# Optimization experiments

Measured on AMD Instinct MI355X. Metric: run time of the kernel, lower is better.

Reference implementation:

```python
import jax, jax.numpy as jnp
import numpy as np
from jax import lax

NUM_NEURONS = 144
NUM_E = 115  # int(144 * 0.8)
NEURONS_PER_CELL = 16
TAU = 2.0
V_TH = 1.0

# action -> (dx, dy) -> grid cell -> neuron slice; precomputed 5x144 current table
_ACTION_TO_POS = {0: (1, 0), 1: (0, -1), 2: (-1, 0), 3: (0, 1), 4: (0, 0)}

def _build_action_table():
    tab = np.zeros((5, NUM_NEURONS), dtype=np.float32)
    for a, (dx, dy) in _ACTION_TO_POS.items():
        x, y = 1 + dx, 1 + dy
        if 0 <= x < 3 and 0 <= y < 3:
            cell = y * 3 + x
            tab[a, cell * NEURONS_PER_CELL:(cell + 1) * NEURONS_PER_CELL] = 5.0
    return jnp.asarray(tab)

_EI_MASK = jnp.concatenate([jnp.ones(NUM_E, jnp.float32), -jnp.ones(NUM_NEURONS - NUM_E, jnp.float32)])


def setup_inputs() -> dict:
    key = jax.random.key(0)
    k1, k2, k3, k4 = jax.random.split(key, 4)
    B, NB = 16384, 8
    actions = jax.random.randint(k1, (B,), 0, 5)
    neighbor_E_spikes = (jax.random.uniform(k2, (B, NB, NUM_E)) < 0.2).astype(jnp.float32)
    W_rec = jax.random.normal(k3, (NUM_NEURONS, NUM_NEURONS), jnp.float32) * 0.01
    mask = jax.random.uniform(jax.random.fold_in(k3, 1), (NUM_NEURONS, NUM_NEURONS)) >= 0.9
    W_rec = W_rec * mask.astype(jnp.float32)
    W_inh = jax.random.normal(k4, (NUM_NEURONS, NUM_E), jnp.float32) * 0.1
    return {"actions": actions, "neighbor_E_spikes": neighbor_E_spikes,
            "W_rec": W_rec, "W_inh": W_inh, "num_ticks": 30}


def reference(actions, neighbor_E_spikes, W_rec, W_inh, num_ticks):
    B = actions.shape[0]
    input_current = _build_action_table()[actions]  # [B, 144]
    # neighbor loop == sum over neighbors, constant across ticks
    inhibition = jnp.einsum('bne,oe->bo', neighbor_E_spikes, W_inh)  # [B, 144]
    const_drive = 0.5 * input_current - 0.5 * inhibition

    def step(carry, _):
        v, acc = carry
        rec = (acc @ W_rec.T) * _EI_MASK          # recurrent input with Dale mask
        x = const_drive + 0.3 * rec
        v = v + (x - v) / TAU                      # LIF charge (decay_input=True, v_reset=0)
        s = (v >= V_TH).astype(v.dtype)            # spike
        v = v * (1.0 - s)                          # hard reset to 0
        return (v, acc + s), None

    init = (jnp.zeros((B, NUM_NEURONS), jnp.float32), jnp.zeros((B, NUM_NEURONS), jnp.float32))
    (_, acc), _ = lax.scan(step, init, None, length=num_ticks)
    return acc[:, :NUM_E]
```

## Files before the change

### kernel.cpp

```cpp
#include <hip/hip_runtime.h>
#include <string.h>


#define NN 144
#define NE 115
#define NB 64
#define RPW 9
#define THREADS 1024

#define CSR_BYTE_OFF 4096

__device__ __forceinline__ float u2f(unsigned u) {
    float f; memcpy(&f, &u, 4); return f;
}

__global__ void prep_kernel(const float* __restrict__ W_rec,
                            int* __restrict__ wsI, char* __restrict__ wsB) {
    __shared__ int cnt[NN];
    __shared__ int rp[NN + 1];
    int t = threadIdx.x;

    if (t < NN) {
        int c = 0;
        for (int j = 0; j < NN; ++j) c += (W_rec[t * NN + j] != 0.0f);
        cnt[t] = c;
    }
    __syncthreads();
    if (t == 0) {
        int s = 0; rp[0] = 0;
        for (int o = 0; o < NN; ++o) { s += (cnt[o] + 3) & ~3; rp[o + 1] = s; }
    }
    __syncthreads();
    if (t <= NN) wsI[t] = rp[t];
    char* base = wsB + CSR_BYTE_OFF;
    if (t < NN) {
        int p = rp[t];
        for (int j = 0; j < NN; ++j) {
            float w = W_rec[t * NN + j];
            if (w != 0.0f) {
                *(unsigned*)(base + 8 * (size_t)p) = (unsigned)j * 256u;
                *(float*)(base + 8 * (size_t)p + 4) = w;
                ++p;
            }
        }
        for (; p < rp[t + 1]; ++p) {
            *(unsigned*)(base + 8 * (size_t)p)  = 0u;
            *(float*)(base + 8 * (size_t)p + 4) = 0.0f;
        }
    }
    if (t < 16) {
        int p = rp[NN] + t;
        *(unsigned*)(base + 8 * (size_t)p)  = 0u;
        *(float*)(base + 8 * (size_t)p + 4) = 0.0f;
    }
}

#define GFMA4(S0, S1)                                                   \
    {                                                                   \
        float a0 = *(const float*)(RbB + ((S0).x + laneB));             \
        float a1 = *(const float*)(RbB + ((S0).z + laneB));             \
        float a2 = *(const float*)(RbB + ((S1).x + laneB));             \
        float a3 = *(const float*)(RbB + ((S1).z + laneB));             \
        rec += (double)u2f((S0).y) * (double)a0;                        \
        rec += (double)u2f((S0).w) * (double)a1;                        \
        rec += (double)u2f((S1).y) * (double)a2;                        \
        rec += (double)u2f((S1).w) * (double)a3;                        \
    }

__global__ __launch_bounds__(THREADS) void snn_kernel(
        const int*   __restrict__ actions,
        const float* __restrict__ spk,
        const float* __restrict__ W_inh,
        const int*   __restrict__ wsI,
        const uint4* __restrict__ csrQ,
        const int*   __restrict__ nt_ptr,
        float*       __restrict__ out,
        int B) {
    __shared__ float accF[2][NN * NB];
    __shared__ int   rpL[NN + 1];

    float* nbF = (float*)&accF[1][0];

    const int t    = threadIdx.x;
    const int lane = t & 63;
    const int wid  = t >> 6;
    const int b0   = blockIdx.x * NB;
    const int b    = b0 + lane;
    const int ticks = *nt_ptr;
    const int R0   = wid * RPW;
    const unsigned laneB = (unsigned)lane * 4u;

    int vz;
    asm volatile("v_mov_b32 %0, 0" : "=v"(vz));

    if (t <= NN) rpL[t] = wsI[t];

    for (int p = t; p < NB * NE; p += THREADS) {
        int bb = p / NE;
        int e  = p - bb * NE;
        float s = 0.0f;
        if (b0 + bb < B) {
            const float* sp = spk + ((size_t)(b0 + bb) * 8) * NE + e;
            #pragma unroll
            for (int n = 0; n < 8; ++n) s += sp[n * NE];
        }
        nbF[e * (NB + 1) + bb] = s;
    }
    for (int i = t; i < NN * NB; i += THREADS) accF[0][i] = 0.0f;
    __syncthreads();

    const int R0s = __builtin_amdgcn_readfirstlane(R0);
    double drv[RPW];
    {
        int a = (b < B) ? actions[b] : 4;
        int cell = (a == 0) ? 5 : (a == 1) ? 1 : (a == 2) ? 3 : (a == 3) ? 7 : 4;
        int cs = cell * 16;
        #pragma unroll
        for (int r = 0; r < RPW; ++r) {
            double inh = 0.0;
            for (int e = 0; e < NE; ++e)
                inh += (double)nbF[e * (NB + 1) + lane]
                     * (double)W_inh[(R0s + r) * NE + e];
            int o = R0 + r;
            double ic = (o >= cs && o < cs + 16) ? 5.0 : 0.0;
            drv[r] = 0.5 * ic - 0.5 * inh;
        }
    }

    int sk0[RPW], sk1[RPW];
    #pragma unroll
    for (int r = 0; r < RPW; ++r) {
        sk0[r] = __builtin_amdgcn_readfirstlane(rpL[R0 + r]);
        sk1[r] = __builtin_amdgcn_readfirstlane(rpL[R0 + r + 1]);
    }
    const uint4* pBase = csrQ + (sk0[0] >> 1) + vz;

    double v[RPW];
    float  accv[RPW];
    #pragma unroll
    for (int r = 0; r < RPW; ++r) { v[r] = 0.0; accv[r] = 0.0f; }

    for (int tk = 0; tk < ticks; ++tk) {
        __syncthreads();
        const float* __restrict__ Rb = accF[tk & 1];
        float*       __restrict__ Wb = accF[(tk & 1) ^ 1];
        const char*  RbB = (const char*)Rb;

        const uint4* p = pBase;
        uint4 SA0 = p[0], SA1 = p[1];
        uint4 SB0 = p[2], SB1 = p[3];

        #pragma unroll
        for (int r = 0; r < RPW; ++r) {
            const int o = R0 + r;
            double rec = 0.0;
            int k = sk0[r];
            const int kend = sk1[r];
            while (k + 8 <= kend) {
                GFMA4(SA0, SA1);
                SA0 = p[4]; SA1 = p[5];
                GFMA4(SB0, SB1);
                SB0 = p[6]; SB1 = p[7];
                p += 4; k += 8;
            }
            if (k < kend) {
                GFMA4(SA0, SA1);
                SA0 = SB0; SA1 = SB1;
                SB0 = p[4]; SB1 = p[5];
                p += 2;
            }
            double x = drv[r] + 0.3 * ((o < NE) ? rec : -rec);
            double vv = v[r];
            vv += (x - vv) * 0.5;
            double s = (vv >= 1.0) ? 1.0 : 0.0;
            vv *= (1.0 - s);
            v[r] = vv;
            accv[r] += (float)s;
            Wb[(o << 6) + lane] = accv[r];
        }
    }

    if (b < B) {
        #pragma unroll
        for (int r = 0; r < RPW; ++r) {
            int o = R0 + r;
            if (o < NE) out[(size_t)b * NE + o] = accv[r];
        }
    }
}

extern "C" void kernel_launch(void* const* d_in, const int* in_sizes, int n_in,
                              void* d_out, int out_size, void* d_ws, size_t ws_size,
                              hipStream_t stream) {
    const int*   actions = (const int*)  d_in[0];
    const float* spk     = (const float*)d_in[1];
    const float* W_rec   = (const float*)d_in[2];
    const float* W_inh   = (const float*)d_in[3];
    const int*   nt      = (const int*)  d_in[4];
    float* out = (float*)d_out;
    int B = in_sizes[0];

    int*  wsI = (int*)d_ws;
    char* wsB = (char*)d_ws;
    const uint4* csrQ = (const uint4*)(wsB + CSR_BYTE_OFF);

    prep_kernel<<<1, 256, 0, stream>>>(W_rec, wsI, wsB);
    int nblocks = (B + NB - 1) / NB;
    snn_kernel<<<nblocks, THREADS, 0, stream>>>(actions, spk, W_inh, wsI, csrQ,
                                                nt, out, B);
}
```

Measured before the change: 362.0 us.

## Accumulate recurrent input incrementally from per-tick spike ballot masks

The recurrent term is now updated incrementally: each tick's spikes are packed into 64-bit ballot masks, one per neuron, stored in shared memory. Each weight is then selected per lane with v_cndmask against the uniform mask, replacing the per-lane gather of the accumulated-spike matrix. This removes the large double-buffered float accumulator from LDS and turns scattered LDS reads into broadcast reads. It also adds two partial sums for more instruction-level parallelism. The costs are readfirstlane and cndmask overhead per nonzero, a reordered tick structure that does one unused sparse pass on the last tick, and a slightly different floating-point summation order.

```diff
diff --git a/kernel.cpp b/kernel.cpp
--- a/kernel.cpp
+++ b/kernel.cpp
@@ -38,7 +38,7 @@
         for (int j = 0; j < NN; ++j) {
             float w = W_rec[t * NN + j];
             if (w != 0.0f) {
-                *(unsigned*)(base + 8 * (size_t)p) = (unsigned)j * 256u;
+                *(unsigned*)(base + 8 * (size_t)p) = (unsigned)j * 8u;
                 *(float*)(base + 8 * (size_t)p + 4) = w;
                 ++p;
             }
@@ -55,16 +55,25 @@
     }
 }
 
-#define GFMA4(S0, S1)                                                   \
+__device__ __forceinline__ float selw(float w, unsigned mlo, unsigned mhi) {
+    unsigned long long mu =
+        (((unsigned long long)(unsigned)__builtin_amdgcn_readfirstlane((int)mhi)) << 32) |
+        (unsigned)__builtin_amdgcn_readfirstlane((int)mlo);
+    float r;
+    asm("v_cndmask_b32 %0, 0, %1, %2" : "=v"(r) : "v"(w), "s"(mu));
+    return r;
+}
+
+#define MSEL4(S0, S1)                                                   \
     {                                                                   \
-        float a0 = *(const float*)(RbB + ((S0).x + laneB));             \
-        float a1 = *(const float*)(RbB + ((S0).z + laneB));             \
-        float a2 = *(const float*)(RbB + ((S1).x + laneB));             \
-        float a3 = *(const float*)(RbB + ((S1).z + laneB));             \
-        rec += (double)u2f((S0).y) * (double)a0;                        \
-        rec += (double)u2f((S0).w) * (double)a1;                        \
-        rec += (double)u2f((S1).y) * (double)a2;                        \
-        rec += (double)u2f((S1).w) * (double)a3;                        \
+        uint2 m0 = *(const uint2*)(mkB + ((S0).x + mOff));              \
+        uint2 m1 = *(const uint2*)(mkB + ((S0).z + mOff));              \
+        uint2 m2 = *(const uint2*)(mkB + ((S1).x + mOff));              \
+        uint2 m3 = *(const uint2*)(mkB + ((S1).z + mOff));              \
+        rec0 += (double)selw(u2f((S0).y), m0.x, m0.y);                  \
+        rec1 += (double)selw(u2f((S0).w), m1.x, m1.y);                  \
+        rec0 += (double)selw(u2f((S1).y), m2.x, m2.y);                  \
+        rec1 += (double)selw(u2f((S1).w), m3.x, m3.y);                  \
     }
 
 __global__ __launch_bounds__(THREADS) void snn_kernel(
@@ -76,10 +85,11 @@
         const int*   __restrict__ nt_ptr,
         float*       __restrict__ out,
         int B) {
-    __shared__ float accF[2][NN * NB];
+    __shared__ unsigned long long maskL[2][NN];
+    __shared__ float nbF[NE][NB + 1];
     __shared__ int   rpL[NN + 1];
 
-    float* nbF = (float*)&accF[1][0];
+    const char* mkB = (const char*)maskL;
 
     const int t    = threadIdx.x;
     const int lane = t & 63;
@@ -88,7 +98,6 @@
     const int b    = b0 + lane;
     const int ticks = *nt_ptr;
     const int R0   = wid * RPW;
-    const unsigned laneB = (unsigned)lane * 4u;
 
     int vz;
     asm volatile("v_mov_b32 %0, 0" : "=v"(vz));
@@ -104,9 +113,8 @@
             #pragma unroll
             for (int n = 0; n < 8; ++n) s += sp[n * NE];
         }
-        nbF[e * (NB + 1) + bb] = s;
-    }
-    for (int i = t; i < NN * NB; i += THREADS) accF[0][i] = 0.0f;
+        nbF[e][bb] = s;
+    }
     __syncthreads();
 
     const int R0s = __builtin_amdgcn_readfirstlane(R0);
@@ -119,8 +127,7 @@
         for (int r = 0; r < RPW; ++r) {
             double inh = 0.0;
             for (int e = 0; e < NE; ++e)
-                inh += (double)nbF[e * (NB + 1) + lane]
-                     * (double)W_inh[(R0s + r) * NE + e];
+                inh += (double)nbF[e][lane] * (double)W_inh[(R0s + r) * NE + e];
             int o = R0 + r;
             double ic = (o >= cs && o < cs + 16) ? 5.0 : 0.0;
             drv[r] = 0.5 * ic - 0.5 * inh;
@@ -135,48 +142,51 @@
     }
     const uint4* pBase = csrQ + (sk0[0] >> 1) + vz;
 
-    double v[RPW];
+    double v[RPW], REC[RPW];
     float  accv[RPW];
     #pragma unroll
-    for (int r = 0; r < RPW; ++r) { v[r] = 0.0; accv[r] = 0.0f; }
+    for (int r = 0; r < RPW; ++r) { v[r] = 0.0; REC[r] = 0.0; accv[r] = 0.0f; }
 
     for (int tk = 0; tk < ticks; ++tk) {
+        #pragma unroll
+        for (int r = 0; r < RPW; ++r) {
+            const int o = R0 + r;
+            double rec = REC[r];
+            double x = drv[r] + 0.3 * ((o < NE) ? rec : -rec);
+            double vv = v[r];
+            vv += (x - vv) * 0.5;
+            bool sp = (vv >= 1.0);
+            unsigned long long m = __ballot(sp);
+            if (lane == r) maskL[tk & 1][R0 + r] = m;
+            v[r] = sp ? 0.0 : vv;
+            accv[r] += sp ? 1.0f : 0.0f;
+        }
         __syncthreads();
-        const float* __restrict__ Rb = accF[tk & 1];
-        float*       __restrict__ Wb = accF[(tk & 1) ^ 1];
-        const char*  RbB = (const char*)Rb;
-
+
+        const unsigned mOff = (unsigned)((tk & 1) * (NN * 8));
         const uint4* p = pBase;
         uint4 SA0 = p[0], SA1 = p[1];
         uint4 SB0 = p[2], SB1 = p[3];
 
         #pragma unroll
         for (int r = 0; r < RPW; ++r) {
-            const int o = R0 + r;
-            double rec = 0.0;
+            double rec0 = 0.0, rec1 = 0.0;
             int k = sk0[r];
             const int kend = sk1[r];
             while (k + 8 <= kend) {
-                GFMA4(SA0, SA1);
+                MSEL4(SA0, SA1);
                 SA0 = p[4]; SA1 = p[5];
-                GFMA4(SB0, SB1);
+                MSEL4(SB0, SB1);
                 SB0 = p[6]; SB1 = p[7];
                 p += 4; k += 8;
             }
             if (k < kend) {
-                GFMA4(SA0, SA1);
+                MSEL4(SA0, SA1);
                 SA0 = SB0; SA1 = SB1;
                 SB0 = p[4]; SB1 = p[5];
                 p += 2;
             }
-            double x = drv[r] + 0.3 * ((o < NE) ? rec : -rec);
-            double vv = v[r];
-            vv += (x - vv) * 0.5;
-            double s = (vv >= 1.0) ? 1.0 : 0.0;
-            vv *= (1.0 - s);
-            v[r] = vv;
-            accv[r] += (float)s;
-            Wb[(o << 6) + lane] = accv[r];
+            REC[r] += rec0 + rec1;
         }
     }
 
```

New measurement: 479.1 us. 32.3% more time.

## Pair rows by sorted nonzero count and split wave halves across paired rows

Applied to the files above, without the earlier changes.

Rows of the sparse recurrent matrix are sorted by nonzero count and paired. Each wave's two 32-lane halves process the two rows of a pair over 32 batch elements, with the sparse entries interleaved so both halves stream from shared chunks. Pairs are assigned to waves in a snake pattern so per-wave work is balanced, and the block shrinks to 32 batches and 512 threads. This targets the uneven per-row work and wasted padding of the old fixed 9-rows-per-wave CSR layout. The cost is padding each pair to the larger row count and more complex prep metadata.

```diff
diff --git a/kernel.cpp b/kernel.cpp
--- a/kernel.cpp
+++ b/kernel.cpp
@@ -4,21 +4,25 @@
 
 #define NN 144
 #define NE 115
-#define NB 64
-#define RPW 9
-#define THREADS 1024
-
-#define CSR_BYTE_OFF 4096
+#define NB 32
+#define THREADS 512
+#define SLOTS 9
+
+#define STREAM_BASE 4096
+#define META_STRIDE 32
 
 __device__ __forceinline__ float u2f(unsigned u) {
     float f; memcpy(&f, &u, 4); return f;
 }
 
 __global__ void prep_kernel(const float* __restrict__ W_rec,
-                            int* __restrict__ wsI, char* __restrict__ wsB) {
-    __shared__ int cnt[NN];
-    __shared__ int rp[NN + 1];
-    int t = threadIdx.x;
+                            int* __restrict__ meta, char* __restrict__ wsB) {
+    __shared__ int cnt[NN], sorted[NN];
+    __shared__ int pkp[72], pOff[72];
+    __shared__ int wBase[8];
+    const int t = threadIdx.x;
+
+    for (int i = t; i < 28672 / 4; i += 256) ((int*)(wsB + STREAM_BASE))[i] = 0;
 
     if (t < NN) {
         int c = 0;
@@ -26,41 +30,67 @@
         cnt[t] = c;
     }
     __syncthreads();
+    if (t < NN) {
+        int ct = cnt[t], r = 0;
+        for (int j = 0; j < NN; ++j) {
+            int cj = cnt[j];
+            r += (cj > ct) || (cj == ct && j < t);
+        }
+        sorted[r] = t;
+    }
+    __syncthreads();
     if (t == 0) {
-        int s = 0; rp[0] = 0;
-        for (int o = 0; o < NN; ++o) { s += (cnt[o] + 3) & ~3; rp[o + 1] = s; }
-    }
-    __syncthreads();
-    if (t <= NN) wsI[t] = rp[t];
-    char* base = wsB + CSR_BYTE_OFF;
-    if (t < NN) {
-        int p = rp[t];
+        int wsum[8][SLOTS];
+        for (int i = 0; i < 72; ++i) {
+            int c0 = cnt[sorted[2 * i]], c1 = cnt[sorted[2 * i + 1]];
+            int mx = c0 > c1 ? c0 : c1; if (mx < 1) mx = 1;
+            pkp[i] = (mx + 3) & ~3;
+            int r = i / 8, pos = i % 8;
+            int w = (r & 1) ? (7 - pos) : pos;
+            wsum[w][r] = i;
+        }
+        int off = 0;
+        for (int w = 0; w < 8; ++w) {
+            wBase[w] = off;
+            for (int r = 0; r < SLOTS; ++r) {
+                int p = wsum[w][r];
+                pOff[p] = off;
+                off += pkp[p] * 16;
+            }
+            for (int r = 0; r < SLOTS; ++r) {
+                int p = wsum[w][r];
+                meta[w * META_STRIDE + 1 + r * 3]     = pkp[p];
+                meta[w * META_STRIDE + 1 + r * 3 + 1] = sorted[2 * p];
+                meta[w * META_STRIDE + 1 + r * 3 + 2] = sorted[2 * p + 1];
+            }
+            meta[w * META_STRIDE] = wBase[w];
+        }
+    }
+    __syncthreads();
+    if (t < 144) {
+        int i = t >> 1, h = t & 1;
+        int row = sorted[2 * i + h];
+        char* base = wsB + STREAM_BASE + pOff[i] + h * 32;
+        int k = 0;
         for (int j = 0; j < NN; ++j) {
-            float w = W_rec[t * NN + j];
+            float w = W_rec[row * NN + j];
             if (w != 0.0f) {
-                *(unsigned*)(base + 8 * (size_t)p) = (unsigned)j * 256u;
-                *(float*)(base + 8 * (size_t)p + 4) = w;
-                ++p;
-            }
-        }
-        for (; p < rp[t + 1]; ++p) {
-            *(unsigned*)(base + 8 * (size_t)p)  = 0u;
-            *(float*)(base + 8 * (size_t)p + 4) = 0.0f;
-        }
-    }
-    if (t < 16) {
-        int p = rp[NN] + t;
-        *(unsigned*)(base + 8 * (size_t)p)  = 0u;
-        *(float*)(base + 8 * (size_t)p + 4) = 0.0f;
-    }
-}
-
-#define GFMA4(S0, S1)                                                   \
+                int c = k >> 2, pos = k & 3;
+                char* a = base + c * 64 + (pos >= 2 ? 16 : 0) + (pos & 1) * 8;
+                *(unsigned*)a     = (unsigned)j * 128u;
+                *(float*)(a + 4)  = w;
+                ++k;
+            }
+        }
+    }
+}
+
+#define GF4(S0, S1)                                                     \
     {                                                                   \
-        float a0 = *(const float*)(RbB + ((S0).x + laneB));             \
-        float a1 = *(const float*)(RbB + ((S0).z + laneB));             \
-        float a2 = *(const float*)(RbB + ((S1).x + laneB));             \
-        float a3 = *(const float*)(RbB + ((S1).z + laneB));             \
+        float a0 = *(const float*)(ldsB + ((S0).x + lro));              \
+        float a1 = *(const float*)(ldsB + ((S0).z + lro));              \
+        float a2 = *(const float*)(ldsB + ((S1).x + lro));              \
+        float a3 = *(const float*)(ldsB + ((S1).z + lro));              \
         rec += (double)u2f((S0).y) * (double)a0;                        \
         rec += (double)u2f((S0).w) * (double)a1;                        \
         rec += (double)u2f((S1).y) * (double)a2;                        \
@@ -71,119 +101,119 @@
         const int*   __restrict__ actions,
         const float* __restrict__ spk,
         const float* __restrict__ W_inh,
-        const int*   __restrict__ wsI,
-        const uint4* __restrict__ csrQ,
+        const int*   __restrict__ meta,
+        const char*  __restrict__ wsB,
         const int*   __restrict__ nt_ptr,
         float*       __restrict__ out,
         int B) {
     __shared__ float accF[2][NN * NB];
-    __shared__ int   rpL[NN + 1];
-
-    float* nbF = (float*)&accF[1][0];
+    __shared__ int   metaL[8 * META_STRIDE];
+
+    const char* ldsB = (const char*)&accF[0][0];
+    float*      nbF  = &accF[1][0];
 
     const int t    = threadIdx.x;
     const int lane = t & 63;
     const int wid  = t >> 6;
+    const int h    = lane >> 5;
+    const int bb   = lane & 31;
     const int b0   = blockIdx.x * NB;
-    const int b    = b0 + lane;
+    const int b    = b0 + bb;
     const int ticks = *nt_ptr;
-    const int R0   = wid * RPW;
-    const unsigned laneB = (unsigned)lane * 4u;
 
     int vz;
     asm volatile("v_mov_b32 %0, 0" : "=v"(vz));
 
-    if (t <= NN) rpL[t] = wsI[t];
+    if (t < 8 * META_STRIDE) metaL[t] = meta[t];
 
     for (int p = t; p < NB * NE; p += THREADS) {
-        int bb = p / NE;
-        int e  = p - bb * NE;
+        int bb2 = p / NE;
+        int e   = p - bb2 * NE;
         float s = 0.0f;
-        if (b0 + bb < B) {
-            const float* sp = spk + ((size_t)(b0 + bb) * 8) * NE + e;
+        if (b0 + bb2 < B) {
+            const float* sp = spk + ((size_t)(b0 + bb2) * 8) * NE + e;
             #pragma unroll
             for (int n = 0; n < 8; ++n) s += sp[n * NE];
         }
-        nbF[e * (NB + 1) + bb] = s;
+        nbF[e * NB + bb2] = s;
     }
     for (int i = t; i < NN * NB; i += THREADS) accF[0][i] = 0.0f;
     __syncthreads();
 
-    const int R0s = __builtin_amdgcn_readfirstlane(R0);
-    double drv[RPW];
+    const int mBase = wid * META_STRIDE;
+    const int sbase = __builtin_amdgcn_readfirstlane(metaL[mBase]);
+    int skp[SLOTS], rows[SLOTS];
+    #pragma unroll
+    for (int r = 0; r < SLOTS; ++r) {
+        skp[r]  = __builtin_amdgcn_readfirstlane(metaL[mBase + 1 + r * 3]);
+        rows[r] = metaL[mBase + 1 + r * 3 + 1 + h];
+    }
+
+    double drv[SLOTS];
     {
         int a = (b < B) ? actions[b] : 4;
-        int cell = (a == 0) ? 5 : (a == 1) ? 1 : (a == 2) ? 3 : (a == 3) ? 7 : 4;
-        int cs = cell * 16;
+        int cs = ((a == 0) ? 5 : (a == 1) ? 1 : (a == 2) ? 3 : (a == 3) ? 7 : 4) * 16;
         #pragma unroll
-        for (int r = 0; r < RPW; ++r) {
+        for (int r = 0; r < SLOTS; ++r) {
             double inh = 0.0;
             for (int e = 0; e < NE; ++e)
-                inh += (double)nbF[e * (NB + 1) + lane]
-                     * (double)W_inh[(R0s + r) * NE + e];
-            int o = R0 + r;
-            double ic = (o >= cs && o < cs + 16) ? 5.0 : 0.0;
+                inh += (double)nbF[e * NB + bb] * (double)W_inh[rows[r] * NE + e];
+            double ic = (rows[r] >= cs && rows[r] < cs + 16) ? 5.0 : 0.0;
             drv[r] = 0.5 * ic - 0.5 * inh;
         }
     }
 
-    int sk0[RPW], sk1[RPW];
+    const uint4* pBase = (const uint4*)(wsB + STREAM_BASE + sbase) + (h << 1) + vz;
+
+    double v[SLOTS];
+    float  accv[SLOTS];
     #pragma unroll
-    for (int r = 0; r < RPW; ++r) {
-        sk0[r] = __builtin_amdgcn_readfirstlane(rpL[R0 + r]);
-        sk1[r] = __builtin_amdgcn_readfirstlane(rpL[R0 + r + 1]);
-    }
-    const uint4* pBase = csrQ + (sk0[0] >> 1) + vz;
-
-    double v[RPW];
-    float  accv[RPW];
-    #pragma unroll
-    for (int r = 0; r < RPW; ++r) { v[r] = 0.0; accv[r] = 0.0f; }
+    for (int r = 0; r < SLOTS; ++r) { v[r] = 0.0; accv[r] = 0.0f; }
 
     for (int tk = 0; tk < ticks; ++tk) {
         __syncthreads();
-        const float* __restrict__ Rb = accF[tk & 1];
-        float*       __restrict__ Wb = accF[(tk & 1) ^ 1];
-        const char*  RbB = (const char*)Rb;
-
-        const uint4* p = pBase;
-        uint4 SA0 = p[0], SA1 = p[1];
-        uint4 SB0 = p[2], SB1 = p[3];
+        const unsigned rbOff = (tk & 1) ? 18432u : 0u;
+        const unsigned lro   = (unsigned)(bb * 4) + rbOff;
+        char* WbB = (char*)ldsB + ((tk & 1) ? 0u : 18432u);
+
+        const uint4* q = pBase;
+        uint4 SA0 = q[0], SA1 = q[1];
+        uint4 SB0 = q[4], SB1 = q[5];
 
         #pragma unroll
-        for (int r = 0; r < RPW; ++r) {
-            const int o = R0 + r;
+        for (int r = 0; r < SLOTS; ++r) {
             double rec = 0.0;
-            int k = sk0[r];
-            const int kend = sk1[r];
+            int k = 0;
+            const int kend = skp[r];
             while (k + 8 <= kend) {
-                GFMA4(SA0, SA1);
-                SA0 = p[4]; SA1 = p[5];
-                GFMA4(SB0, SB1);
-                SB0 = p[6]; SB1 = p[7];
-                p += 4; k += 8;
+                GF4(SA0, SA1);
+                SA0 = q[8];  SA1 = q[9];
+                GF4(SB0, SB1);
+                SB0 = q[12]; SB1 = q[13];
+                q += 8; k += 8;
             }
             if (k < kend) {
-                GFMA4(SA0, SA1);
+                GF4(SA0, SA1);
                 SA0 = SB0; SA1 = SB1;
-                SB0 = p[4]; SB1 = p[5];
-                p += 2;
-            }
+                SB0 = q[8]; SB1 = q[9];
+                q += 4;
+            }
+            const int o = rows[r];
             double x = drv[r] + 0.3 * ((o < NE) ? rec : -rec);
             double vv = v[r];
             vv += (x - vv) * 0.5;
-            double s = (vv >= 1.0) ? 1.0 : 0.0;
-            vv *= (1.0 - s);
+            double sd = (vv >= 1.0) ? 1.0 : 0.0;
+            vv *= (1.0 - sd);
             v[r] = vv;
-            accv[r] += (float)s;
-            Wb[(o << 6) + lane] = accv[r];
+            accv[r] += (float)sd;
+            *(float*)(WbB + (unsigned)o * 128u + bb * 4) = accv[r];
         }
     }
 
     if (b < B) {
         #pragma unroll
-        for (int r = 0; r < RPW; ++r) {
-            int o = R0 + r;
+        for (int r = 0; r < SLOTS; ++r) {
+            int o = rows[r];
             if (o < NE) out[(size_t)b * NE + o] = accv[r];
         }
     }
@@ -200,12 +230,11 @@
     float* out = (float*)d_out;
     int B = in_sizes[0];
 
-    int*  wsI = (int*)d_ws;
-    char* wsB = (char*)d_ws;
-    const uint4* csrQ = (const uint4*)(wsB + CSR_BYTE_OFF);
-
-    prep_kernel<<<1, 256, 0, stream>>>(W_rec, wsI, wsB);
+    int*  meta = (int*)d_ws;
+    char* wsB  = (char*)d_ws;
+
+    prep_kernel<<<1, 256, 0, stream>>>(W_rec, meta, wsB);
     int nblocks = (B + NB - 1) / NB;
-    snn_kernel<<<nblocks, THREADS, 0, stream>>>(actions, spk, W_inh, wsI, csrQ,
+    snn_kernel<<<nblocks, THREADS, 0, stream>>>(actions, spk, W_inh, meta, wsB,
                                                 nt, out, B);
 }
```

After: 403.4 us. 1.11x slower.
